# Kernel optimization log

Measured on AMD Instinct MI355X. Metric: run time of the kernel, lower is better.

Reference implementation:

```python
import jax, jax.numpy as jnp
import numpy as np

ADJ = np.array([[0,1,0,0,0,0],[1,0,1,0,1,0],[0,1,0,1,0,0],[0,0,1,0,0,0],[0,1,0,0,0,1],[0,0,0,0,1,0]])
EDGES = np.stack(np.nonzero(ADJ), axis=1)  # [10,2] row-major, same order as torch.nonzero
UPPER = (1, 2, 3, 4)
N_PART = 6
B, H, W = 1, 96, 96


def conv1x1(x, w):
    return jnp.einsum('bchw,oc->bohw', x, w)


def affine(x, s, b):  # InPlaceABNSync(activation='none'), eval mode with stats folded into scale/bias
    return x * s[None, :, None, None] + b[None, :, None, None]


def bilinear(x, py, px):  # x [B,C,H,W]; py,px [B,H,W]; zero padding outside
    Hh, Ww = x.shape[2], x.shape[3]
    def samp(img, py, px):
        y0 = jnp.floor(py); x0 = jnp.floor(px)
        wy = py - y0; wx = px - x0
        def get(yi, xi):
            valid = ((yi >= 0) & (yi < Hh) & (xi >= 0) & (xi < Ww)).astype(img.dtype)
            yc = jnp.clip(yi, 0, Hh - 1).astype(jnp.int32)
            xc = jnp.clip(xi, 0, Ww - 1).astype(jnp.int32)
            return img[:, yc, xc] * valid
        return (get(y0, x0) * (1 - wy) * (1 - wx) + get(y0, x0 + 1) * (1 - wy) * wx
                + get(y0 + 1, x0) * wy * (1 - wx) + get(y0 + 1, x0 + 1) * wy * wx)
    return jax.vmap(samp)(x, py, px)


def dfconv(x, ow, ob, w):
    # modulated deformable conv v2 (DCNv2), 3x3, stride 1, pad 1, 1 deformable group
    o = jax.lax.conv_general_dilated(x, ow, (1, 1), 'SAME',
            dimension_numbers=('NCHW', 'OIHW', 'NCHW')) + ob[None, :, None, None]
    off, mask = o[:, :18], jax.nn.sigmoid(o[:, 18:27])
    Hh, Ww = x.shape[2], x.shape[3]
    yy, xx = jnp.meshgrid(jnp.arange(Hh, dtype=x.dtype), jnp.arange(Ww, dtype=x.dtype), indexing='ij')
    out = jnp.zeros((x.shape[0], w.shape[0], Hh, Ww), x.dtype)
    for k in range(9):  # fixed 3x3 taps
        py = yy[None] + (k // 3 - 1) + off[:, 2 * k]
        px = xx[None] + (k % 3 - 1) + off[:, 2 * k + 1]
        s = bilinear(x, py, px) * mask[:, k:k + 1]
        out = out + jnp.einsum('bchw,oc->bohw', s, w[:, :, k // 3, k % 3])
    return out


def gru_cell(x, h, wih, bih, whh, bhh):  # Conv2dGRU cell, 1x1 kernel, single step
    gi = conv1x1(x, wih) + bih[None, :, None, None]
    gh = conv1x1(h, whh) + bhh[None, :, None, None]
    i_r, i_z, i_n = jnp.split(gi, 3, axis=1)
    h_r, h_z, h_n = jnp.split(gh, 3, axis=1)
    r = jax.nn.sigmoid(i_r + h_r)
    z = jax.nn.sigmoid(i_z + h_z)
    n = jnp.tanh(i_n + r * h_n)
    return (1 - z) * n + z * h


def _forward(p_fea, xp, xh, dp_ow1, dp_ob1, dp_w1, dp_s1, dp_b1, dp_ow2, dp_ob2, dp_w2, dp_s2, dp_b2,
             dp_aw, dp_ab, dp_bw, dp_bb, dc_w1, dc_s1, dc_b1, dc_w2, dc_b2, dc_wfh, dc_sfh, dc_bfh,
             gru_wih1, gru_bih1, gru_whh1, gru_bhh1, gru_wih2, gru_bih2, gru_whh2, gru_bhh2):
    # Part_Dependency per directed edge (A -> B)
    per_node = [[] for _ in range(N_PART)]
    for e in range(EDGES.shape[0]):
        a, b = int(EDGES[e, 0]), int(EDGES[e, 1])
        pA, pB = xp[a], xp[b]
        h = jax.nn.relu(affine(dfconv(jnp.concatenate([p_fea, pA], 1), dp_ow1[e], dp_ob1[e], dp_w1[e]), dp_s1[e], dp_b1[e]))
        h = jax.nn.relu(affine(dfconv(h, dp_ow2[e], dp_ob2[e], dp_w2[e]), dp_s2[e], dp_b2[e]))
        A_att = jax.nn.sigmoid(conv1x1(pA, dp_aw[e]) + dp_ab[e][None, :, None, None])
        B_att = jax.nn.sigmoid(conv1x1(pB, dp_bw[e]) + dp_bb[e][None, :, None, None])
        per_node[b].append((1 - A_att) * h * B_att)
    # max-aggregation of incoming messages per part node
    xpp = [m[0] if len(m) == 1 else jnp.max(jnp.stack(m, -1), -1) for m in per_node]
    # decomp: half-node -> part-node messages, then sum
    msgs = []
    for j in range(N_PART):
        hf = xh[0] if (j + 1) in UPPER else xh[1]
        cat = jnp.concatenate([hf, xp[j]], 1)
        a_ = jax.nn.relu(affine(conv1x1(cat, dc_w1[j]), dc_s1[j], dc_b1[j]))
        att = jax.nn.sigmoid(conv1x1(a_, dc_w2[j]) + dc_b2[j][None, :, None, None])
        xhp = jax.nn.relu(affine(conv1x1(att * p_fea, dc_wfh[j]), dc_sfh[j], dc_bfh[j]))
        msgs.append(xpp[j] + xhp)
    # per-node 2-layer Conv2dGRU update (seq len 1, h0 = 0); take layer-2 hidden
    xp_out = []
    h0 = jnp.zeros_like(xp[0])
    for j in range(N_PART):
        xin = jnp.concatenate([xp[j], msgs[j]], 1)
        h1 = gru_cell(xin, h0, gru_wih1[j], gru_bih1[j], gru_whh1[j], gru_bhh1[j])
        h2 = gru_cell(h1, h0, gru_wih2[j], gru_bih2[j], gru_whh2[j], gru_bhh2[j])
        xp_out.append(h2)
    return jnp.stack(xp_out, 0), jnp.stack(msgs, 0)


def setup_inputs():
    ks = iter(jax.random.split(jax.random.key(0), 64))
    nrm = lambda shape, s: jax.random.normal(next(ks), shape, jnp.float32) * s
    HD, IN, E = 10, 256, EDGES.shape[0]
    N = N_PART
    return {
        'p_fea': nrm((B, IN, H, W), 1.0),
        'xp': nrm((N, B, HD, H, W), 1.0),
        'xh': nrm((2, B, HD, H, W), 1.0),
        'dp_ow1': nrm((E, 27, IN + HD, 3, 3), 0.005), 'dp_ob1': nrm((E, 27), 0.01),
        'dp_w1': nrm((E, 2 * HD, IN + HD, 3, 3), 0.02),
        'dp_s1': jnp.ones((E, 2 * HD), jnp.float32), 'dp_b1': jnp.zeros((E, 2 * HD), jnp.float32),
        'dp_ow2': nrm((E, 27, 2 * HD, 3, 3), 0.02), 'dp_ob2': nrm((E, 27), 0.01),
        'dp_w2': nrm((E, HD, 2 * HD, 3, 3), 0.07),
        'dp_s2': jnp.ones((E, HD), jnp.float32), 'dp_b2': jnp.zeros((E, HD), jnp.float32),
        'dp_aw': nrm((E, 1, HD), 0.3), 'dp_ab': jnp.zeros((E, 1), jnp.float32),
        'dp_bw': nrm((E, 1, HD), 0.3), 'dp_bb': jnp.zeros((E, 1), jnp.float32),
        'dc_w1': nrm((N, 2 * HD, 2 * HD), 0.2),
        'dc_s1': jnp.ones((N, 2 * HD), jnp.float32), 'dc_b1': jnp.zeros((N, 2 * HD), jnp.float32),
        'dc_w2': nrm((N, 1, 2 * HD), 0.2), 'dc_b2': jnp.zeros((N, 1), jnp.float32),
        'dc_wfh': nrm((N, HD, IN), 0.06),
        'dc_sfh': jnp.ones((N, HD), jnp.float32), 'dc_bfh': jnp.zeros((N, HD), jnp.float32),
        'gru_wih1': nrm((N, 3 * HD, 2 * HD), 0.2), 'gru_bih1': jnp.zeros((N, 3 * HD), jnp.float32),
        'gru_whh1': nrm((N, 3 * HD, HD), 0.3), 'gru_bhh1': jnp.zeros((N, 3 * HD), jnp.float32),
        'gru_wih2': nrm((N, 3 * HD, HD), 0.3), 'gru_bih2': jnp.zeros((N, 3 * HD), jnp.float32),
        'gru_whh2': nrm((N, 3 * HD, HD), 0.3), 'gru_bhh2': jnp.zeros((N, 3 * HD), jnp.float32),
    }


def reference(p_fea, xp, xh, dp_ow1, dp_ob1, dp_w1, dp_s1, dp_b1, dp_ow2, dp_ob2, dp_w2, dp_s2, dp_b2,
              dp_aw, dp_ab, dp_bw, dp_bb, dc_w1, dc_s1, dc_b1, dc_w2, dc_b2, dc_wfh, dc_sfh, dc_bfh,
              gru_wih1, gru_bih1, gru_whh1, gru_bhh1, gru_wih2, gru_bih2, gru_whh2, gru_bhh2):
    return _forward(p_fea, xp, xh, dp_ow1, dp_ob1, dp_w1, dp_s1, dp_b1, dp_ow2, dp_ob2, dp_w2, dp_s2, dp_b2,
                    dp_aw, dp_ab, dp_bw, dp_bb, dc_w1, dc_s1, dc_b1, dc_w2, dc_b2, dc_wfh, dc_sfh, dc_bfh,
                    gru_wih1, gru_bih1, gru_whh1, gru_bhh1, gru_wih2, gru_bih2, gru_whh2, gru_bhh2)
```

## Files before the change

### kernel.cpp

```cpp
#include <hip/hip_runtime.h>
#include <hip/hip_bf16.h>

#define DEV static __device__ __forceinline__

DEV float sigm(float x) { return 1.f / (1.f + __expf(-x)); }

typedef __attribute__((ext_vector_type(8))) short s8;
typedef __attribute__((ext_vector_type(4))) float f4;
typedef _Float16 h4 __attribute__((ext_vector_type(4)));

DEV unsigned short f2bf(float f) {
  unsigned u = __float_as_uint(f);
  return (unsigned short)((u + 0x7FFFu + ((u >> 16) & 1u)) >> 16);
}
DEV float bf2f(unsigned short h) { return __uint_as_float(((unsigned)h) << 16); }

__constant__ int d_esrc[10] = {0,1,1,1,2,2,3,4,4,5};
__constant__ int d_inc[6][3] = {{1,-1,-1},{0,4,7},{2,6,-1},{5,-1,-1},{3,9,-1},{8,-1,-1}};
__constant__ int d_ne[6] = {1,3,2,1,2,1};

#define TW 32
#define TH 8
#define SW 41
#define SDC 40
#define SH 16
#define SN 656

DEV void prep_w_body(const float* src, float* dst, int OC, int C,
                     int tap_major, int total, int i) {
  if (i >= total) return;
  int t = i % 9; int n = i / 9;
  int c = n % C; n /= C;
  int oc = n % OC; int e = n / OC;
  float v = src[i];
  int inner = tap_major ? (t * C + c) : (c * 9 + t);
  dst[(e * C * 9 + inner) * OC + oc] = v;
}

__global__ void prep_all_k(const float* __restrict__ dp_ow2, float* __restrict__ wf2,
                           const float* __restrict__ dp_w2, float* __restrict__ wm2,
                           const float* __restrict__ dp_ow1,
                           unsigned short* __restrict__ aw1,
                           const float* __restrict__ dp_w1,
                           unsigned short* __restrict__ awY,
                           unsigned short* __restrict__ awU, int use_u) {
  int b = blockIdx.x;
  if (b < 190) {
    prep_w_body(dp_ow2, wf2, 27, 20, 0, 48600, b * 256 + threadIdx.x);
  } else if (b < 261) {
    prep_w_body(dp_w2, wm2, 10, 20, 1, 18000, (b - 190) * 256 + threadIdx.x);
  } else if (b < 926) {
    if (use_u) return;
    int i = (b - 261) * 256 + threadIdx.x;
    if (i >= 170240) return;
    int lane = i & 63;
    int tile = (i >> 6) & 1;
    int cg = (i >> 7) % 133;
    int e = (i >> 7) / 133;
    int m = lane & 15, quad = lane >> 4;
    int oc = tile * 16 + m;
    unsigned short* out = aw1 + ((e * 133 + cg) * 2 + tile) * 1024 + lane * 16;
#pragma unroll
    for (int j = 0; j < 8; ++j) {
      int k = quad * 8 + j;
      int csel = k >> 4, t = k & 15;
      int c = 2 * cg + csel;
      float w = (oc < 27 && t < 9) ? dp_ow1[((e * 27 + oc) * 266 + c) * 9 + t] : 0.f;
      unsigned short h = f2bf(w);
      out[j] = h;
      out[8 + j] = f2bf(w - bf2f(h));
    }
  } else if (b < 1196) {
    if (use_u) return;
    int i = (b - 926) * 256 + threadIdx.x;
    int lane = i & 63;
    int grp = i >> 6;
    int mt = grp % 12;
    int ks = (grp / 12) % 9;
    int e = grp / 108;
    int m16 = lane & 15, quad = lane >> 4;
    int M = mt * 16 + m16;
    unsigned short* out = awY + ((e * 9 + ks) * 12 + mt) * 1024 + lane * 16;
#pragma unroll
    for (int j = 0; j < 8; ++j) {
      int c = ks * 32 + quad * 8 + j;
      float w = 0.f;
      if (M < 180 && c < 266) {
        int tap = M / 20, oc = M % 20;
        w = dp_w1[((e * 20 + oc) * 266 + c) * 9 + tap];
      }
      unsigned short h = f2bf(w);
      out[j] = h;
      out[8 + j] = f2bf(w - bf2f(h));
    }
  } else {
    if (!use_u) return;
    int i = (b - 1196) * 256 + threadIdx.x;
    int lane = i & 63;
    int grp = i >> 6;
    int mt = grp % 28;
    int ks = (grp / 28) % 9;
    int e = grp / 252;
    int m16 = lane & 15, quad = lane >> 4;
    int M = mt * 16 + m16;
    unsigned short* out = awU + ((e * 9 + ks) * 28 + mt) * 1024 + lane * 16;
#pragma unroll
    for (int j = 0; j < 8; ++j) {
      int c = ks * 32 + quad * 8 + j;
      float w = 0.f;
      if (c < 266) {
        if (M < 180) {
          int tap = M / 20, oc = M % 20;
          w = dp_w1[((e * 20 + oc) * 266 + c) * 9 + tap];
        } else if (M >= 192 && M < 435) {
          int u = M - 192, tap = u / 27, oc = u % 27;
          w = dp_ow1[((e * 27 + oc) * 266 + c) * 9 + tap];
        }
      }
      unsigned short h = f2bf(w);
      out[j] = h;
      out[8 + j] = f2bf(w - bf2f(h));
    }
  }
}

__global__ void init2_k(const float* __restrict__ ob, float* __restrict__ o2,
                        float* __restrict__ h2) {
  int i = blockIdx.x * 256 + threadIdx.x;
  if (i < 2488320) o2[i] = ob[i / 9216];
  else h2[i - 2488320] = 0.f;
}

DEV int stage_goff(int i, int ty0, int tx0) {
  int r = i / SW, cl = i % SW;
  cl = min(cl, SDC - 1);
  int gy = min(max(ty0 - 4 + r, 0), 95);
  int gx = min(max(tx0 - 4 + cl, 0), 95);
  return gy * 96 + gx;
}

__global__ __launch_bounds__(256) void uni_gemm_k(
    const float* __restrict__ pfea, const float* __restrict__ xp,
    const unsigned short* __restrict__ awU, unsigned short* __restrict__ Yg,
    unsigned short* __restrict__ Ug) {
  const int pxg = blockIdx.x, z = blockIdx.y, e = blockIdx.z;
  const int tid = threadIdx.x;
  const int lane = tid & 63, wv = tid >> 6;
  const int quad = lane >> 4, n16 = lane & 15;
  const float* xpe = xp + d_esrc[e] * 10 * 9216;
  const int qbase = pxg * 256 + wv * 64;

  f4 acc[4][4] = {};

  for (int ks = 0; ks < 9; ++ks) {
    const int cq = ks * 32 + quad * 8;
    s8 Ah[4], Al[4];
#pragma unroll
    for (int mt = 0; mt < 4; ++mt) {
      const unsigned short* ap =
          awU + ((e * 9 + ks) * 28 + z * 4 + mt) * 1024 + lane * 16;
      Ah[mt] = *(const s8*)ap;
      Al[mt] = *(const s8*)(ap + 8);
    }
#pragma unroll
    for (int nt = 0; nt < 4; ++nt) {
      const int q = qbase + nt * 16 + n16;
      union { s8 v; unsigned short u[8]; } Bh;
#pragma unroll
      for (int j = 0; j < 8; ++j) {
        int c = cq + j;
        float v = 0.f;
        if (c < 256) v = pfea[c * 9216 + q];
        else if (c < 266) v = xpe[(c - 256) * 9216 + q];
        Bh.u[j] = f2bf(v);
      }
#pragma unroll
      for (int mt = 0; mt < 4; ++mt) {
        acc[nt][mt] = __builtin_amdgcn_mfma_f32_16x16x32_bf16(Ah[mt], Bh.v, acc[nt][mt], 0, 0, 0);
        acc[nt][mt] = __builtin_amdgcn_mfma_f32_16x16x32_bf16(Al[mt], Bh.v, acc[nt][mt], 0, 0, 0);
      }
    }
  }
  _Float16* Yh = (_Float16*)Yg;
  _Float16* Uh = (_Float16*)Ug;
#pragma unroll
  for (int nt = 0; nt < 4; ++nt) {
    const int q = qbase + nt * 16 + n16;
#pragma unroll
    for (int mt = 0; mt < 4; ++mt)
#pragma unroll
      for (int r = 0; r < 4; ++r) {
        int m = (z * 4 + mt) * 16 + quad * 4 + r;
        if (m < 180) {
          int tap = m / 20, oc = m - tap * 20;
          Yh[((e * 9 + tap) * 9216 + q) * 20 + oc] = (_Float16)acc[nt][mt][r];
        } else if (m >= 192 && m < 435) {
          Uh[(e * 243 + (m - 192)) * 9216 + q] = (_Float16)acc[nt][mt][r];
        }
      }
  }
}

__global__ __launch_bounds__(256) void shiftadd_k(
    const unsigned short* __restrict__ Ug, const float* __restrict__ ob,
    float* __restrict__ o1) {
  const int p = blockIdx.x * 256 + threadIdx.x;
  const int e = blockIdx.y;
  const int y = p / 96, x = p % 96;
  const _Float16* Uh = (const _Float16*)Ug;
  float acc[27];
#pragma unroll
  for (int oc = 0; oc < 27; ++oc) acc[oc] = ob[e * 27 + oc];
#pragma unroll
  for (int t = 0; t < 9; ++t) {
    int yy = y + t / 3 - 1, xx = x + t % 3 - 1;
    if (yy >= 0 && yy < 96 && xx >= 0 && xx < 96) {
      int q = yy * 96 + xx;
      const _Float16* up = Uh + (e * 243 + t * 27) * 9216 + q;
#pragma unroll
      for (int oc = 0; oc < 27; ++oc)
        acc[oc] += (float)up[oc * 9216];
    }
  }
#pragma unroll
  for (int oc = 0; oc < 27; ++oc) o1[(e * 27 + oc) * 9216 + p] = acc[oc];
}

#define OSWB 35
#define OSEC 384
#define OBUF 896

__global__ __launch_bounds__(256) void offconv1_mfma_k(
    const float* __restrict__ pfea, const float* __restrict__ xp,
    const unsigned short* __restrict__ aw, const float* __restrict__ ob,
    float* __restrict__ o1) {
  __shared__ float sbuf[2][OBUF];
  const int e = blockIdx.x, m = blockIdx.y, z = blockIdx.z;
  const int tid = threadIdx.x;
  const int lane = tid & 63, wv = tid >> 6;
  const int quad = lane >> 4, n16 = lane & 15;
  const int tx0 = (m % 3) * 32, ty0 = (m / 3) * 8;
  const float* xpe = xp + d_esrc[e] * 10 * 9216;
  const int cg_lo = (z * 133) / 4, cg_hi = ((z + 1) * 133) / 4;

  int g[3]; bool oks[3];
#pragma unroll
  for (int i = 0; i < 3; ++i) {
    int s = tid + i * 256;
    int sec = s / OSEC, off = s - sec * OSEC;
    int r = off / OSWB, cl = off % OSWB;
    int gy = ty0 - 1 + r, gx = tx0 - 1 + cl;
    bool ok = (off < 350) && (cl < 34) && (gy >= 0) && (gy < 96) &&
              (gx >= 0) && (gx < 96);
    oks[i] = ok;
    g[i] = sec * 9216 + (ok ? (gy * 96 + gx) : 0);
  }
  if (tid < OBUF - 768) { sbuf[0][768 + tid] = 0.f; sbuf[1][768 + tid] = 0.f; }

  const int tbase = (quad & 1) * 8;
  const int csel = quad >> 1;
  int bdelta[8];
#pragma unroll
  for (int j = 0; j < 8; ++j) {
    int t = tbase + j;
    int dy = t / 3 - 1, dx = t % 3 - 1;
    bdelta[j] = csel * OSEC + dy * OSWB + dx;
  }
  int bidx[4];
#pragma unroll
  for (int nt = 0; nt < 4; ++nt) {
    int r = 2 * wv + (nt >> 1), h = nt & 1;
    bidx[nt] = (r + 1) * OSWB + (h * 16 + n16 + 1);
  }

  f4 acc[4][2] = {};

  int c0 = 2 * cg_lo;
  const float* base = (c0 < 256) ? (pfea + c0 * 9216) : (xpe + (c0 - 256) * 9216);
  float pv0 = oks[0] ? base[g[0]] : 0.f;
  float pv1 = oks[1] ? base[g[1]] : 0.f;
  float pv2 = oks[2] ? base[g[2]] : 0.f;

  int bsel = 0;
  for (int cg = cg_lo; cg < cg_hi; ++cg, bsel ^= 1) {
    float* buf = sbuf[bsel];
    buf[tid] = pv0; buf[tid + 256] = pv1; buf[tid + 512] = pv2;
    if (cg + 1 < cg_hi) {
      int c0n = 2 * (cg + 1);
      const float* nb = (c0n < 256) ? (pfea + c0n * 9216)
                                    : (xpe + (c0n - 256) * 9216);
      pv0 = oks[0] ? nb[g[0]] : 0.f;
      pv1 = oks[1] ? nb[g[1]] : 0.f;
      pv2 = oks[2] ? nb[g[2]] : 0.f;
    }
    const unsigned short* apc = aw + (e * 133 + cg) * 2048 + lane * 16;
    s8 Ah0 = *(const s8*)(apc);
    s8 Al0 = *(const s8*)(apc + 8);
    s8 Ah1 = *(const s8*)(apc + 1024);
    s8 Al1 = *(const s8*)(apc + 1024 + 8);
    __syncthreads();
#pragma unroll
    for (int nt = 0; nt < 4; ++nt) {
      union { s8 v; unsigned short u[8]; } Bh, Bl;
#pragma unroll
      for (int j = 0; j < 8; ++j) {
        float v = buf[bidx[nt] + bdelta[j]];
        unsigned short h = f2bf(v);
        Bh.u[j] = h;
        Bl.u[j] = f2bf(v - bf2f(h));
      }
      acc[nt][0] = __builtin_amdgcn_mfma_f32_16x16x32_bf16(Ah0, Bh.v, acc[nt][0], 0, 0, 0);
      acc[nt][0] = __builtin_amdgcn_mfma_f32_16x16x32_bf16(Ah0, Bl.v, acc[nt][0], 0, 0, 0);
      acc[nt][0] = __builtin_amdgcn_mfma_f32_16x16x32_bf16(Al0, Bh.v, acc[nt][0], 0, 0, 0);
      acc[nt][1] = __builtin_amdgcn_mfma_f32_16x16x32_bf16(Ah1, Bh.v, acc[nt][1], 0, 0, 0);
      acc[nt][1] = __builtin_amdgcn_mfma_f32_16x16x32_bf16(Ah1, Bl.v, acc[nt][1], 0, 0, 0);
      acc[nt][1] = __builtin_amdgcn_mfma_f32_16x16x32_bf16(Al1, Bh.v, acc[nt][1], 0, 0, 0);
    }
  }
#pragma unroll
  for (int nt = 0; nt < 4; ++nt) {
    int y = ty0 + 2 * wv + (nt >> 1);
    int xx = tx0 + (nt & 1) * 16 + n16;
    int p = y * 96 + xx;
#pragma unroll
    for (int t2 = 0; t2 < 2; ++t2)
#pragma unroll
      for (int r = 0; r < 4; ++r) {
        int oc = t2 * 16 + quad * 4 + r;
        if (oc < 27) {
          float v = acc[nt][t2][r];
          if (z == 0) v += ob[e * 27 + oc];
          atomicAdd(&o1[(e * 27 + oc) * 9216 + p], v);
        }
      }
  }
}

__global__ __launch_bounds__(256) void ygemm_k(
    const float* __restrict__ pfea, const float* __restrict__ xp,
    const unsigned short* __restrict__ awY, unsigned short* __restrict__ Yg) {
  const int pxg = blockIdx.x, z = blockIdx.y, e = blockIdx.z;
  const int tid = threadIdx.x;
  const int lane = tid & 63, wv = tid >> 6;
  const int quad = lane >> 4, n16 = lane & 15;
  const float* xpe = xp + d_esrc[e] * 10 * 9216;
  const int qbase = pxg * 256 + wv * 64;

  f4 acc[4][3] = {};

  for (int ks = 0; ks < 9; ++ks) {
    const int cq = ks * 32 + quad * 8;
    s8 Ah[3], Al[3];
#pragma unroll
    for (int mt = 0; mt < 3; ++mt) {
      const unsigned short* ap =
          awY + ((e * 9 + ks) * 12 + z * 3 + mt) * 1024 + lane * 16;
      Ah[mt] = *(const s8*)ap;
      Al[mt] = *(const s8*)(ap + 8);
    }
#pragma unroll
    for (int nt = 0; nt < 4; ++nt) {
      const int q = qbase + nt * 16 + n16;
      union { s8 v; unsigned short u[8]; } Bh, Bl;
#pragma unroll
      for (int j = 0; j < 8; ++j) {
        int c = cq + j;
        float v = 0.f;
        if (c < 256) v = pfea[c * 9216 + q];
        else if (c < 266) v = xpe[(c - 256) * 9216 + q];
        unsigned short h = f2bf(v);
        Bh.u[j] = h;
        Bl.u[j] = f2bf(v - bf2f(h));
      }
#pragma unroll
      for (int mt = 0; mt < 3; ++mt) {
        acc[nt][mt] = __builtin_amdgcn_mfma_f32_16x16x32_bf16(Ah[mt], Bh.v, acc[nt][mt], 0, 0, 0);
        acc[nt][mt] = __builtin_amdgcn_mfma_f32_16x16x32_bf16(Ah[mt], Bl.v, acc[nt][mt], 0, 0, 0);
        acc[nt][mt] = __builtin_amdgcn_mfma_f32_16x16x32_bf16(Al[mt], Bh.v, acc[nt][mt], 0, 0, 0);
      }
    }
  }
  _Float16* Yh = (_Float16*)Yg;
#pragma unroll
  for (int nt = 0; nt < 4; ++nt) {
    const int q = qbase + nt * 16 + n16;
#pragma unroll
    for (int mt = 0; mt < 3; ++mt)
#pragma unroll
      for (int r = 0; r < 4; ++r) {
        int m = z * 48 + mt * 16 + quad * 4 + r;
        if (m < 180) {
          int tap = m / 20, oc = m - tap * 20;
          Yh[((e * 9 + tap) * 9216 + q) * 20 + oc] = (_Float16)acc[nt][mt][r];
        }
      }
  }
}

__global__ __launch_bounds__(256) void dfgather_k(
    const float* __restrict__ o1, const unsigned short* __restrict__ Yg,
    float* __restrict__ h1a) {
  const int p = blockIdx.x * 256 + threadIdx.x;
  const int zt = blockIdx.y, e = blockIdx.z;
  const int y = p / 96, x = p % 96;
  float acc[20];
#pragma unroll
  for (int oc = 0; oc < 20; ++oc) acc[oc] = 0.f;

  const _Float16* Yh = (const _Float16*)Yg;
#pragma unroll
  for (int t = 0; t < 3; ++t) {
    const int k = zt * 3 + t;
    float offy = o1[(e * 27 + 2 * k) * 9216 + p];
    float offx = o1[(e * 27 + 2 * k + 1) * 9216 + p];
    float mk = sigm(o1[(e * 27 + 18 + k) * 9216 + p]);
    float py = (float)(y + k / 3 - 1) + offy;
    float px = (float)(x + k % 3 - 1) + offx;
    float fy = floorf(py), fx = floorf(px);
    float wy = py - fy, wx = px - fx;
    int iy = (int)fy, ix = (int)fx;
    const _Float16* yk = Yh + (e * 9 + k) * 9216 * 20;
#pragma unroll
    for (int dy = 0; dy < 2; ++dy)
#pragma unroll
      for (int dx = 0; dx < 2; ++dx) {
        bool ok = (iy + dy >= 0) && (iy + dy < 96) && (ix + dx >= 0) && (ix + dx < 96);
        float cwc = (ok ? mk : 0.f) * (dy ? wy : (1.f - wy)) * (dx ? wx : (1.f - wx));
        int yc = min(max(iy + dy, 0), 95), xc = min(max(ix + dx, 0), 95);
        const h4* yp = (const h4*)(yk + (yc * 96 + xc) * 20);
#pragma unroll
        for (int g = 0; g < 5; ++g) {
          h4 v = yp[g];
#pragma unroll
          for (int u = 0; u < 4; ++u)
            acc[g * 4 + u] = fmaf(cwc, (float)v[u], acc[g * 4 + u]);
        }
      }
  }
#pragma unroll
  for (int oc = 0; oc < 20; ++oc)
    atomicAdd(&h1a[(e * 20 + oc) * 9216 + p], acc[oc]);
}

__global__ __launch_bounds__(256) void offconv2_k(
    const float* __restrict__ h1a, const float* __restrict__ wf,
    const float* __restrict__ s1, const float* __restrict__ b1,
    float* __restrict__ o2) {
  __shared__ float sbuf[2][2 * SN];
  const int e = blockIdx.x, m = blockIdx.y;
  const int c_lo = blockIdx.z * 10;
  const int tid = threadIdx.x;
  const int tx = tid % TW, ty = tid / TW;
  const int tx0 = (m % 3) * TW, ty0 = (m / 3) * TH;
  const int y = ty0 + ty, x = tx0 + tx;
  const int p = y * 96 + x;
  const float* base = h1a + e * 20 * 9216;

  const int g0 = stage_goff(tid, ty0, tx0);
  const int g1 = stage_goff(tid + 256, ty0, tx0);
  const int g2 = (tid < SN - 512) ? stage_goff(tid + 512, ty0, tx0) : 0;

  float vmask[9];
#pragma unroll
  for (int t = 0; t < 9; ++t) {
    int yy = y + t / 3 - 1, xx = x + t % 3 - 1;
    vmask[t] = ((yy >= 0) && (yy < 96) && (xx >= 0) && (xx < 96)) ? 1.f : 0.f;
  }
  const int vbase = (ty + 3) * SW + (tx + 3);

  float acc[27];
#pragma unroll
  for (int oc = 0; oc < 27; ++oc) acc[oc] = 0.f;

  const float* ia = base + c_lo * 9216;
  const float* ib = ia + 9216;
  float pa0 = ia[g0], pa1 = ia[g1], pa2 = (tid < SN - 512) ? ia[g2] : 0.f;
  float pb0 = ib[g0], pb1 = ib[g1], pb2 = (tid < SN - 512) ? ib[g2] : 0.f;

  int bsel = 0;
  for (int c = c_lo; c < c_lo + 10; c += 2, bsel ^= 1) {
    float sa = s1[e * 20 + c], ba = b1[e * 20 + c];
    float sb = s1[e * 20 + c + 1], bb2 = b1[e * 20 + c + 1];
    float* buf = sbuf[bsel];
    buf[tid] = fmaxf(fmaf(sa, pa0, ba), 0.f);
    buf[tid + 256] = fmaxf(fmaf(sa, pa1, ba), 0.f);
    if (tid < SN - 512) buf[tid + 512] = fmaxf(fmaf(sa, pa2, ba), 0.f);
    buf[SN + tid] = fmaxf(fmaf(sb, pb0, bb2), 0.f);
    buf[SN + tid + 256] = fmaxf(fmaf(sb, pb1, bb2), 0.f);
    if (tid < SN - 512) buf[SN + tid + 512] = fmaxf(fmaf(sb, pb2, bb2), 0.f);
    if (c + 2 < c_lo + 10) {
      const float* na = base + (c + 2) * 9216;
      const float* nb = base + (c + 3) * 9216;
      pa0 = na[g0]; pa1 = na[g1]; if (tid < SN - 512) pa2 = na[g2];
      pb0 = nb[g0]; pb1 = nb[g1]; if (tid < SN - 512) pb2 = nb[g2];
    }
    __syncthreads();
#pragma unroll
    for (int cc = 0; cc < 2; ++cc) {
      const float* wc = wf + (e * 20 + c + cc) * 243;
      const float* bp = buf + cc * SN;
#pragma unroll
      for (int t = 0; t < 9; ++t) {
        float v = vmask[t] * bp[vbase + (t / 3) * SW + (t % 3)];
#pragma unroll
        for (int oc = 0; oc < 27; ++oc)
          acc[oc] = fmaf(v, wc[t * 27 + oc], acc[oc]);
      }
    }
  }
#pragma unroll
  for (int oc = 0; oc < 27; ++oc)
    atomicAdd(&o2[(e * 27 + oc) * 9216 + p], acc[oc]);
}

__global__ __launch_bounds__(256) void dfmain2_k(
    const float* __restrict__ h1a, const float* __restrict__ o2,
    const float* __restrict__ wm, const float* __restrict__ s1,
    const float* __restrict__ b1, float* __restrict__ hout) {
  __shared__ float sbuf[2][2 * SN];
  const int e = blockIdx.x, m = blockIdx.y;
  const int c_lo = blockIdx.z * 10;
  const int tid = threadIdx.x;
  const int tx = tid % TW, ty = tid / TW;
  const int tx0 = (m % 3) * TW, ty0 = (m / 3) * TH;
  const int y = ty0 + ty, x = tx0 + tx;
  const int p = y * 96 + x;
  const float* base = h1a + e * 20 * 9216;

  const int g0 = stage_goff(tid, ty0, tx0);
  const int g1 = stage_goff(tid + 256, ty0, tx0);
  const int g2 = (tid < SN - 512) ? stage_goff(tid + 512, ty0, tx0) : 0;

  int iob[9]; float cw[9][4];
  bool oob = false;
#pragma unroll
  for (int k = 0; k < 9; ++k) {
    float offy = o2[(e * 27 + 2 * k) * 9216 + p];
    float offx = o2[(e * 27 + 2 * k + 1) * 9216 + p];
    float mk = sigm(o2[(e * 27 + 18 + k) * 9216 + p]);
    float py = (float)(y + k / 3 - 1) + offy;
    float px = (float)(x + k % 3 - 1) + offx;
    float fy = floorf(py), fx = floorf(px);
    float wy = py - fy, wx = px - fx;
    int iy = (int)fy, ix = (int)fx;
#pragma unroll
    for (int dy = 0; dy < 2; ++dy)
#pragma unroll
      for (int dx = 0; dx < 2; ++dx) {
        bool ok = (iy + dy >= 0) && (iy + dy < 96) && (ix + dx >= 0) && (ix + dx < 96);
        cw[k][dy * 2 + dx] =
            (ok ? mk : 0.f) * (dy ? wy : (1.f - wy)) * (dx ? wx : (1.f - wx));
      }
    int ir = iy - (ty0 - 4), ic = ix - (tx0 - 4);
    oob |= ((unsigned)ir > (unsigned)(SH - 2)) | ((unsigned)ic > (unsigned)(SDC - 2));
    iob[k] = min(max(ir, 0), SH - 2) * SW + min(max(ic, 0), SDC - 2);
  }

  float acc[10];
#pragma unroll
  for (int oc = 0; oc < 10; ++oc) acc[oc] = 0.f;

  const float* ia = base + c_lo * 9216;
  const float* ib = ia + 9216;
  float pa0 = ia[g0], pa1 = ia[g1], pa2 = (tid < SN - 512) ? ia[g2] : 0.f;
  float pb0 = ib[g0], pb1 = ib[g1], pb2 = (tid < SN - 512) ? ib[g2] : 0.f;

  int bsel = 0;
  for (int c = c_lo; c < c_lo + 10; c += 2, bsel ^= 1) {
    float sa = s1[e * 20 + c], ba = b1[e * 20 + c];
    float sb = s1[e * 20 + c + 1], bb2 = b1[e * 20 + c + 1];
    float* buf = sbuf[bsel];
    buf[tid] = fmaxf(fmaf(sa, pa0, ba), 0.f);
    buf[tid + 256] = fmaxf(fmaf(sa, pa1, ba), 0.f);
    if (tid < SN - 512) buf[tid + 512] = fmaxf(fmaf(sa, pa2, ba), 0.f);
    buf[SN + tid] = fmaxf(fmaf(sb, pb0, bb2), 0.f);
    buf[SN + tid + 256] = fmaxf(fmaf(sb, pb1, bb2), 0.f);
    if (tid < SN - 512) buf[SN + tid + 512] = fmaxf(fmaf(sb, pb2, bb2), 0.f);
    if (c + 2 < c_lo + 10) {
      const float* na = base + (c + 2) * 9216;
      const float* nb = base + (c + 3) * 9216;
      pa0 = na[g0]; pa1 = na[g1]; if (tid < SN - 512) pa2 = na[g2];
      pb0 = nb[g0]; pb1 = nb[g1]; if (tid < SN - 512) pb2 = nb[g2];
    }
    __syncthreads();
#pragma unroll
    for (int cc = 0; cc < 2; ++cc) {
      const float* bp = buf + cc * SN;
#pragma unroll
      for (int k = 0; k < 9; ++k) {
        const float* bk = bp + iob[k];
        float sv = cw[k][0] * bk[0] + cw[k][1] * bk[1] +
                   cw[k][2] * bk[SW] + cw[k][3] * bk[SW + 1];
        const float* wc = wm + ((e * 9 + k) * 20 + c + cc) * 10;
#pragma unroll
        for (int oc = 0; oc < 10; ++oc) acc[oc] = fmaf(sv, wc[oc], acc[oc]);
      }
    }
  }

  if (oob) {
#pragma unroll
    for (int oc = 0; oc < 10; ++oc) acc[oc] = 0.f;
    for (int k = 0; k < 9; ++k) {
      float offy = o2[(e * 27 + 2 * k) * 9216 + p];
      float offx = o2[(e * 27 + 2 * k + 1) * 9216 + p];
      float mk = sigm(o2[(e * 27 + 18 + k) * 9216 + p]);
      float py = (float)(y + k / 3 - 1) + offy;
      float px = (float)(x + k % 3 - 1) + offx;
      float fy = floorf(py), fx = floorf(px);
      float wy = py - fy, wx = px - fx;
      int iy = (int)fy, ix = (int)fx;
      int go[4]; float gw[4];
#pragma unroll
      for (int dy = 0; dy < 2; ++dy)
#pragma unroll
        for (int dx = 0; dx < 2; ++dx) {
          bool ok = (iy + dy >= 0) && (iy + dy < 96) && (ix + dx >= 0) && (ix + dx < 96);
          int yc = min(max(iy + dy, 0), 95), xc = min(max(ix + dx, 0), 95);
          go[dy * 2 + dx] = yc * 96 + xc;
          gw[dy * 2 + dx] =
              (ok ? mk : 0.f) * (dy ? wy : (1.f - wy)) * (dx ? wx : (1.f - wx));
        }
      for (int c = c_lo; c < c_lo + 10; ++c) {
        float sc = s1[e * 20 + c], bc = b1[e * 20 + c];
        const float* ptr = base + c * 9216;
        float v0 = fmaxf(fmaf(sc, ptr[go[0]], bc), 0.f);
        float v1 = fmaxf(fmaf(sc, ptr[go[1]], bc), 0.f);
        float v2 = fmaxf(fmaf(sc, ptr[go[2]], bc), 0.f);
        float v3 = fmaxf(fmaf(sc, ptr[go[3]], bc), 0.f);
        float sv = gw[0] * v0 + gw[1] * v1 + gw[2] * v2 + gw[3] * v3;
        const float* wc = wm + ((e * 9 + k) * 20 + c) * 10;
#pragma unroll
        for (int oc = 0; oc < 10; ++oc) acc[oc] = fmaf(sv, wc[oc], acc[oc]);
      }
    }
  }
#pragma unroll
  for (int oc = 0; oc < 10; ++oc)
    atomicAdd(&hout[(e * 10 + oc) * 9216 + p], acc[oc]);
}

__global__ __launch_bounds__(256) void conv_fh_k(
    const float* __restrict__ pfea, const float* __restrict__ wfh,
    float* __restrict__ accfh) {
  const int j = blockIdx.y;
  const int z = blockIdx.z;
  const int p = blockIdx.x * 256 + threadIdx.x;
  const int c_lo = z * 64;
  float acc[10];
#pragma unroll
  for (int c = 0; c < 10; ++c) acc[c] = 0.f;
  for (int ci = c_lo; ci < c_lo + 64; ci += 4) {
    float pv0 = pfea[ci * 9216 + p];
    float pv1 = pfea[(ci + 1) * 9216 + p];
    float pv2 = pfea[(ci + 2) * 9216 + p];
    float pv3 = pfea[(ci + 3) * 9216 + p];
#pragma unroll
    for (int c = 0; c < 10; ++c) {
      acc[c] = fmaf(pv0, wfh[(j * 10 + c) * 256 + ci], acc[c]);
      acc[c] = fmaf(pv1, wfh[(j * 10 + c) * 256 + ci + 1], acc[c]);
      acc[c] = fmaf(pv2, wfh[(j * 10 + c) * 256 + ci + 2], acc[c]);
      acc[c] = fmaf(pv3, wfh[(j * 10 + c) * 256 + ci + 3], acc[c]);
    }
  }
#pragma unroll
  for (int c = 0; c < 10; ++c)
    atomicAdd(&accfh[(j * 10 + c) * 9216 + p], acc[c]);
}

__global__ __launch_bounds__(256) void msggru_k(
    const float* __restrict__ xp, const float* __restrict__ xh,
    const float* __restrict__ h2, const float* __restrict__ accfh,
    const float* __restrict__ s2, const float* __restrict__ b2g,
    const float* __restrict__ aw, const float* __restrict__ ab,
    const float* __restrict__ bw, const float* __restrict__ bb,
    const float* __restrict__ w1, const float* __restrict__ s1,
    const float* __restrict__ b1, const float* __restrict__ w2,
    const float* __restrict__ b2, const float* __restrict__ sfh,
    const float* __restrict__ bfh,
    const float* __restrict__ wih1, const float* __restrict__ bih1,
    const float* __restrict__ bhh1, const float* __restrict__ wih2,
    const float* __restrict__ bih2, const float* __restrict__ bhh2,
    float* __restrict__ out_m, float* __restrict__ out_x) {
  const int j = blockIdx.y;
  const int p = blockIdx.x * 256 + threadIdx.x;
  float xj[10];
#pragma unroll
  for (int c = 0; c < 10; ++c) xj[c] = xp[(j * 10 + c) * 9216 + p];
  float xpp[10];
  int ne = d_ne[j];
  for (int ei = 0; ei < ne; ++ei) {
    int e = d_inc[j][ei];
    int a2 = d_esrc[e];
    float sA = ab[e];
#pragma unroll
    for (int c = 0; c < 10; ++c)
      sA = fmaf(xp[(a2 * 10 + c) * 9216 + p], aw[e * 10 + c], sA);
    float sB = bb[e];
#pragma unroll
    for (int c = 0; c < 10; ++c) sB = fmaf(xj[c], bw[e * 10 + c], sB);
    float f = (1.f - sigm(sA)) * sigm(sB);
#pragma unroll
    for (int c = 0; c < 10; ++c) {
      float raw = h2[(e * 10 + c) * 9216 + p];
      float hv = fmaxf(fmaf(s2[e * 10 + c], raw, b2g[e * 10 + c]), 0.f);
      float mm = f * hv;
      xpp[c] = (ei == 0) ? mm : fmaxf(xpp[c], mm);
    }
  }
  const float* hf = xh + ((j < 4) ? 0 : 1) * 10 * 9216;
  float cat[20];
#pragma unroll
  for (int c = 0; c < 10; ++c) cat[c] = hf[c * 9216 + p];
#pragma unroll
  for (int c = 0; c < 10; ++c) cat[10 + c] = xj[c];
  float at = b2[j];
#pragma unroll
  for (int oc = 0; oc < 20; ++oc) {
    float t = 0.f;
#pragma unroll
    for (int c = 0; c < 20; ++c)
      t = fmaf(cat[c], w1[(j * 20 + oc) * 20 + c], t);
    float av = fmaxf(s1[j * 20 + oc] * t + b1[j * 20 + oc], 0.f);
    at = fmaf(av, w2[j * 20 + oc], at);
  }
  at = sigm(at);
  float msg[10];
#pragma unroll
  for (int c = 0; c < 10; ++c) {
    float xhp = fmaxf(sfh[j * 10 + c] * (at * accfh[(j * 10 + c) * 9216 + p]) +
                          bfh[j * 10 + c], 0.f);
    msg[c] = xpp[c] + xhp;
    out_m[(j * 10 + c) * 9216 + p] = msg[c];
  }
  float gi[30];
#pragma unroll
  for (int r = 0; r < 30; ++r) gi[r] = bih1[j * 30 + r];
#pragma unroll
  for (int c = 0; c < 10; ++c) {
    float v = xj[c];
#pragma unroll
    for (int r = 0; r < 30; ++r)
      gi[r] = fmaf(v, wih1[(j * 30 + r) * 20 + c], gi[r]);
  }
#pragma unroll
  for (int c = 0; c < 10; ++c) {
    float v = msg[c];
#pragma unroll
    for (int r = 0; r < 30; ++r)
      gi[r] = fmaf(v, wih1[(j * 30 + r) * 20 + 10 + c], gi[r]);
  }
  float h1v[10];
#pragma unroll
  for (int c = 0; c < 10; ++c) {
    float r = sigm(gi[c] + bhh1[j * 30 + c]);
    float z = sigm(gi[10 + c] + bhh1[j * 30 + 10 + c]);
    float n = tanhf(gi[20 + c] + r * bhh1[j * 30 + 20 + c]);
    h1v[c] = (1.f - z) * n;
  }
  float g2v[30];
#pragma unroll
  for (int r = 0; r < 30; ++r) g2v[r] = bih2[j * 30 + r];
#pragma unroll
  for (int c = 0; c < 10; ++c) {
    float v = h1v[c];
#pragma unroll
    for (int r = 0; r < 30; ++r)
      g2v[r] = fmaf(v, wih2[(j * 30 + r) * 10 + c], g2v[r]);
  }
#pragma unroll
  for (int c = 0; c < 10; ++c) {
    float r = sigm(g2v[c] + bhh2[j * 30 + c]);
    float z = sigm(g2v[10 + c] + bhh2[j * 30 + 10 + c]);
    float n = tanhf(g2v[20 + c] + r * bhh2[j * 30 + 20 + c]);
    out_x[(j * 10 + c) * 9216 + p] = (1.f - z) * n;
  }
}

extern "C" void kernel_launch(void* const* d_in, const int* in_sizes, int n_in,
                              void* d_out, int out_size, void* d_ws, size_t ws_size,
                              hipStream_t stream) {
  const float* pfea   = (const float*)d_in[0];
  const float* xp     = (const float*)d_in[1];
  const float* xh     = (const float*)d_in[2];
  const float* dp_ow1 = (const float*)d_in[3];
  const float* dp_ob1 = (const float*)d_in[4];
  const float* dp_w1  = (const float*)d_in[5];
  const float* dp_s1  = (const float*)d_in[6];
  const float* dp_b1  = (const float*)d_in[7];
  const float* dp_ow2 = (const float*)d_in[8];
  const float* dp_ob2 = (const float*)d_in[9];
  const float* dp_w2  = (const float*)d_in[10];
  const float* dp_s1x = dp_s1;
  const float* dp_s2  = (const float*)d_in[11];
  const float* dp_b2  = (const float*)d_in[12];
  const float* dp_aw  = (const float*)d_in[13];
  const float* dp_ab  = (const float*)d_in[14];
  const float* dp_bw  = (const float*)d_in[15];
  const float* dp_bb  = (const float*)d_in[16];
  const float* dc_w1  = (const float*)d_in[17];
  const float* dc_s1  = (const float*)d_in[18];
  const float* dc_b1  = (const float*)d_in[19];
  const float* dc_w2  = (const float*)d_in[20];
  const float* dc_b2  = (const float*)d_in[21];
  const float* dc_wfh = (const float*)d_in[22];
  const float* dc_sfh = (const float*)d_in[23];
  const float* dc_bfh = (const float*)d_in[24];
  const float* g_wih1 = (const float*)d_in[25];
  const float* g_bih1 = (const float*)d_in[26];
  const float* g_bhh1 = (const float*)d_in[28];
  const float* g_wih2 = (const float*)d_in[29];
  const float* g_bih2 = (const float*)d_in[30];
  const float* g_bhh2 = (const float*)d_in[32];
  (void)dp_s1x;

  float* ws = (float*)d_ws;
  const bool use_u = ws_size >= 26654760ull * sizeof(float);

  unsigned short *aw1, *awY = nullptr, *awU = nullptr, *Yg, *Ug = nullptr;
  float *accfh, *h2, *wf2, *wm2, *o1, *o2, *h1a;

  if (use_u) {
    aw1   = (unsigned short*)ws;
    accfh = ws;
    h2    = ws + 552960;
    awU   = (unsigned short*)(ws + 1474560);
    wf2   = ws + 1474560 + 1290240;
    wm2   = wf2 + 48600;
    o1    = wm2 + 18000;
    o2    = o1;
    h1a   = o1 + 2488320;
    Yg    = (unsigned short*)(h1a + 1843200);
    Ug    = (unsigned short*)(h1a + 1843200 + 8294400);
  } else {
    aw1   = (unsigned short*)ws;
    awY   = (unsigned short*)(ws + 1361920);
    accfh = ws;
    h2    = ws + 552960;
    wf2   = ws + 1914880;
    wm2   = wf2 + 48600;
    o1    = wm2 + 18000;
    o2    = o1;
    h1a   = o1 + 2488320;
    Yg    = (unsigned short*)(ws + 6313000);
  }

  float* out_x = (float*)d_out;
  float* out_m = out_x + 552960;

  dim3 blk(256);
  prep_all_k<<<dim3(1826), blk, 0, stream>>>(dp_ow2, wf2, dp_w2, wm2,
                                             dp_ow1, aw1, dp_w1, awY ? awY : aw1,
                                             awU ? awU : aw1, use_u ? 1 : 0);

  if (use_u) {
    hipMemsetAsync(h1a, 0, 1843200 * sizeof(float), stream);
    uni_gemm_k<<<dim3(36, 7, 10), blk, 0, stream>>>(pfea, xp, awU, Yg, Ug);
    shiftadd_k<<<dim3(36, 10), blk, 0, stream>>>(Ug, dp_ob1, o1);
    dfgather_k<<<dim3(36, 3, 10), blk, 0, stream>>>(o1, Yg, h1a);
  } else {
    hipMemsetAsync(o1, 0, (2488320 + 1843200) * sizeof(float), stream);
    offconv1_mfma_k<<<dim3(10, 36, 4), blk, 0, stream>>>(pfea, xp, aw1, dp_ob1, o1);
    ygemm_k<<<dim3(36, 4, 10), blk, 0, stream>>>(pfea, xp, awY, Yg);
    dfgather_k<<<dim3(36, 3, 10), blk, 0, stream>>>(o1, Yg, h1a);
  }

  init2_k<<<dim3(13320), blk, 0, stream>>>(dp_ob2, o2, h2);
  offconv2_k<<<dim3(10, 36, 2), blk, 0, stream>>>(h1a, wf2, dp_s1, dp_b1, o2);
  dfmain2_k<<<dim3(10, 36, 2), blk, 0, stream>>>(h1a, o2, wm2, dp_s1, dp_b1, h2);

  hipMemsetAsync(accfh, 0, 552960 * sizeof(float), stream);
  conv_fh_k<<<dim3(36, 6, 4), blk, 0, stream>>>(pfea, dc_wfh, accfh);

  msggru_k<<<dim3(36, 6), blk, 0, stream>>>(
      xp, xh, h2, accfh, dp_s2, dp_b2, dp_aw, dp_ab, dp_bw, dp_bb,
      dc_w1, dc_s1, dc_b1, dc_w2, dc_b2, dc_sfh, dc_bfh,
      g_wih1, g_bih1, g_bhh1, g_wih2, g_bih2, g_bhh2, out_m, out_x);
}
```

Baseline: 417.6 us.

## Pre-transpose GEMM inputs to pixel-major bf16 and vectorize GEMM operand loads and stores

Adds a transpose kernel that converts pfea and the per-node xp channels once into pixel-major bf16 buffers, reusing the o1 workspace region. The unified GEMM then loads each B fragment as a single 16-byte vector instead of eight strided fp32 loads with per-element conversion, work that was repeated across all 70 z/edge blocks. The Y output is now written as a 4-wide half vector. The cost is an extra kernel launch and an extra pass over the input; the buffer aliasing with o1 relies on o1 being written only after the GEMM has finished.

```diff
diff --git a/kernel.cpp b/kernel.cpp
--- a/kernel.cpp
+++ b/kernel.cpp
@@ -124,6 +124,39 @@
   }
 }
 
+__global__ __launch_bounds__(256) void xt_k(
+    const float* __restrict__ pfea, const float* __restrict__ xp,
+    unsigned short* __restrict__ Xt_p, unsigned short* __restrict__ Xt_x) {
+  __shared__ unsigned int lds[256][17];
+  const int q0 = blockIdx.x * 256, yb = blockIdx.y;
+  const int t = threadIdx.x;
+  if (yb < 8) {
+    const int c0 = yb * 32;
+#pragma unroll
+    for (int cc = 0; cc < 32; cc += 2) {
+      float v0 = pfea[(c0 + cc) * 9216 + q0 + t];
+      float v1 = pfea[(c0 + cc + 1) * 9216 + q0 + t];
+      lds[t][cc >> 1] = (unsigned)f2bf(v0) | ((unsigned)f2bf(v1) << 16);
+    }
+    __syncthreads();
+    unsigned int* dst = (unsigned int*)(Xt_p + (size_t)(q0 + t) * 256 + c0);
+#pragma unroll
+    for (int u = 0; u < 16; ++u) dst[u] = lds[t][u];
+  } else {
+    const int node = yb - 8;
+#pragma unroll
+    for (int cc = 0; cc < 32; cc += 2) {
+      float v0 = (cc < 10) ? xp[(node * 10 + cc) * 9216 + q0 + t] : 0.f;
+      float v1 = (cc + 1 < 10) ? xp[(node * 10 + cc + 1) * 9216 + q0 + t] : 0.f;
+      lds[t][cc >> 1] = (unsigned)f2bf(v0) | ((unsigned)f2bf(v1) << 16);
+    }
+    __syncthreads();
+    unsigned int* dst = (unsigned int*)(Xt_x + ((size_t)node * 9216 + q0 + t) * 32);
+#pragma unroll
+    for (int u = 0; u < 16; ++u) dst[u] = lds[t][u];
+  }
+}
+
 __global__ void init2_k(const float* __restrict__ ob, float* __restrict__ o2,
                         float* __restrict__ h2) {
   int i = blockIdx.x * 256 + threadIdx.x;
@@ -140,64 +173,73 @@
 }
 
 __global__ __launch_bounds__(256) void uni_gemm_k(
-    const float* __restrict__ pfea, const float* __restrict__ xp,
+    const unsigned short* __restrict__ Xt_p,
+    const unsigned short* __restrict__ Xt_x,
     const unsigned short* __restrict__ awU, unsigned short* __restrict__ Yg,
     unsigned short* __restrict__ Ug) {
   const int pxg = blockIdx.x, z = blockIdx.y, e = blockIdx.z;
   const int tid = threadIdx.x;
   const int lane = tid & 63, wv = tid >> 6;
   const int quad = lane >> 4, n16 = lane & 15;
-  const float* xpe = xp + d_esrc[e] * 10 * 9216;
+  const unsigned short* xtx = Xt_x + (size_t)d_esrc[e] * 9216 * 32;
   const int qbase = pxg * 256 + wv * 64;
+  int q[4];
+#pragma unroll
+  for (int nt = 0; nt < 4; ++nt) q[nt] = qbase + nt * 16 + n16;
 
   f4 acc[4][4] = {};
 
   for (int ks = 0; ks < 9; ++ks) {
-    const int cq = ks * 32 + quad * 8;
     s8 Ah[4], Al[4];
 #pragma unroll
     for (int mt = 0; mt < 4; ++mt) {
       const unsigned short* ap =
-          awU + ((e * 9 + ks) * 28 + z * 4 + mt) * 1024 + lane * 16;
+          awU + (((size_t)e * 9 + ks) * 28 + z * 4 + mt) * 1024 + lane * 16;
       Ah[mt] = *(const s8*)ap;
       Al[mt] = *(const s8*)(ap + 8);
     }
-#pragma unroll
-    for (int nt = 0; nt < 4; ++nt) {
-      const int q = qbase + nt * 16 + n16;
-      union { s8 v; unsigned short u[8]; } Bh;
-#pragma unroll
-      for (int j = 0; j < 8; ++j) {
-        int c = cq + j;
-        float v = 0.f;
-        if (c < 256) v = pfea[c * 9216 + q];
-        else if (c < 266) v = xpe[(c - 256) * 9216 + q];
-        Bh.u[j] = f2bf(v);
-      }
+    s8 B[4];
+    if (ks < 8) {
+      const int co = ks * 32 + quad * 8;
+#pragma unroll
+      for (int nt = 0; nt < 4; ++nt)
+        B[nt] = *(const s8*)(Xt_p + (size_t)q[nt] * 256 + co);
+    } else {
+      const int co = quad * 8;
+#pragma unroll
+      for (int nt = 0; nt < 4; ++nt)
+        B[nt] = *(const s8*)(xtx + (size_t)q[nt] * 32 + co);
+    }
+#pragma unroll
+    for (int nt = 0; nt < 4; ++nt)
 #pragma unroll
       for (int mt = 0; mt < 4; ++mt) {
-        acc[nt][mt] = __builtin_amdgcn_mfma_f32_16x16x32_bf16(Ah[mt], Bh.v, acc[nt][mt], 0, 0, 0);
-        acc[nt][mt] = __builtin_amdgcn_mfma_f32_16x16x32_bf16(Al[mt], Bh.v, acc[nt][mt], 0, 0, 0);
-      }
-    }
+        acc[nt][mt] = __builtin_amdgcn_mfma_f32_16x16x32_bf16(Ah[mt], B[nt], acc[nt][mt], 0, 0, 0);
+        acc[nt][mt] = __builtin_amdgcn_mfma_f32_16x16x32_bf16(Al[mt], B[nt], acc[nt][mt], 0, 0, 0);
+      }
   }
   _Float16* Yh = (_Float16*)Yg;
   _Float16* Uh = (_Float16*)Ug;
 #pragma unroll
   for (int nt = 0; nt < 4; ++nt) {
-    const int q = qbase + nt * 16 + n16;
-#pragma unroll
-    for (int mt = 0; mt < 4; ++mt)
-#pragma unroll
-      for (int r = 0; r < 4; ++r) {
-        int m = (z * 4 + mt) * 16 + quad * 4 + r;
-        if (m < 180) {
-          int tap = m / 20, oc = m - tap * 20;
-          Yh[((e * 9 + tap) * 9216 + q) * 20 + oc] = (_Float16)acc[nt][mt][r];
-        } else if (m >= 192 && m < 435) {
-          Uh[(e * 243 + (m - 192)) * 9216 + q] = (_Float16)acc[nt][mt][r];
+#pragma unroll
+    for (int mt = 0; mt < 4; ++mt) {
+      int m0 = (z * 4 + mt) * 16 + quad * 4;
+      if (m0 < 180) {
+        int tap = m0 / 20, oc0 = m0 - tap * 20;
+        h4 v;
+#pragma unroll
+        for (int r = 0; r < 4; ++r) v[r] = (_Float16)acc[nt][mt][r];
+        *(h4*)(Yh + (((size_t)(e * 9 + tap)) * 9216 + q[nt]) * 20 + oc0) = v;
+      } else {
+#pragma unroll
+        for (int r = 0; r < 4; ++r) {
+          int m = m0 + r;
+          if (m >= 192 && m < 435)
+            Uh[((size_t)e * 243 + (m - 192)) * 9216 + q[nt]] = (_Float16)acc[nt][mt][r];
         }
       }
+    }
   }
 }
 
@@ -216,7 +258,7 @@
     int yy = y + t / 3 - 1, xx = x + t % 3 - 1;
     if (yy >= 0 && yy < 96 && xx >= 0 && xx < 96) {
       int q = yy * 96 + xx;
-      const _Float16* up = Uh + (e * 243 + t * 27) * 9216 + q;
+      const _Float16* up = Uh + ((size_t)e * 243 + t * 27) * 9216 + q;
 #pragma unroll
       for (int oc = 0; oc < 27; ++oc)
         acc[oc] += (float)up[oc * 9216];
@@ -419,7 +461,7 @@
     float fy = floorf(py), fx = floorf(px);
     float wy = py - fy, wx = px - fx;
     int iy = (int)fy, ix = (int)fx;
-    const _Float16* yk = Yh + (e * 9 + k) * 9216 * 20;
+    const _Float16* yk = Yh + (size_t)(e * 9 + k) * 9216 * 20;
 #pragma unroll
     for (int dy = 0; dy < 2; ++dy)
 #pragma unroll
@@ -791,7 +833,6 @@
   const float* dp_ow2 = (const float*)d_in[8];
   const float* dp_ob2 = (const float*)d_in[9];
   const float* dp_w2  = (const float*)d_in[10];
-  const float* dp_s1x = dp_s1;
   const float* dp_s2  = (const float*)d_in[11];
   const float* dp_b2  = (const float*)d_in[12];
   const float* dp_aw  = (const float*)d_in[13];
@@ -812,12 +853,12 @@
   const float* g_wih2 = (const float*)d_in[29];
   const float* g_bih2 = (const float*)d_in[30];
   const float* g_bhh2 = (const float*)d_in[32];
-  (void)dp_s1x;
 
   float* ws = (float*)d_ws;
   const bool use_u = ws_size >= 26654760ull * sizeof(float);
 
   unsigned short *aw1, *awY = nullptr, *awU = nullptr, *Yg, *Ug = nullptr;
+  unsigned short *Xt_p = nullptr, *Xt_x = nullptr;
   float *accfh, *h2, *wf2, *wm2, *o1, *o2, *h1a;
 
   if (use_u) {
@@ -829,6 +870,8 @@
     wm2   = wf2 + 48600;
     o1    = wm2 + 18000;
     o2    = o1;
+    Xt_p  = (unsigned short*)o1;
+    Xt_x  = Xt_p + 2359296;
     h1a   = o1 + 2488320;
     Yg    = (unsigned short*)(h1a + 1843200);
     Ug    = (unsigned short*)(h1a + 1843200 + 8294400);
@@ -854,8 +897,9 @@
                                              awU ? awU : aw1, use_u ? 1 : 0);
 
   if (use_u) {
+    xt_k<<<dim3(36, 14), blk, 0, stream>>>(pfea, xp, Xt_p, Xt_x);
     hipMemsetAsync(h1a, 0, 1843200 * sizeof(float), stream);
-    uni_gemm_k<<<dim3(36, 7, 10), blk, 0, stream>>>(pfea, xp, awU, Yg, Ug);
+    uni_gemm_k<<<dim3(36, 7, 10), blk, 0, stream>>>(Xt_p, Xt_x, awU, Yg, Ug);
     shiftadd_k<<<dim3(36, 10), blk, 0, stream>>>(Ug, dp_ob1, o1);
     dfgather_k<<<dim3(36, 3, 10), blk, 0, stream>>>(o1, Yg, h1a);
   } else {
```

New measurement: 396.5 us. 1.05x faster.
